# Performance work log

Hardware: AMD Instinct MI355X
Metric: run time of the kernel (lower is better)

The kernel has to match this reference:

```python
import jax, jax.numpy as jnp
import numpy as np

B, L, D, U = 8, 512, 256, 32

def setup_inputs() -> dict:
    key = jax.random.key(0)
    ks = jax.random.split(key, 6)
    g = lambda k, shape: jax.random.normal(k, shape, dtype=jnp.float32) * (2.0 / sum(shape)) ** 0.5
    return {
        "x": jax.random.normal(ks[0], (B, L, D), dtype=jnp.float32),
        "Wt": g(ks[1], (D, U)),
        "Wx": g(ks[2], (D, U)),
        "bh": jnp.zeros((U,), dtype=jnp.float32),
        "Wa": g(ks[3], (U, 1)),
        "ba": jnp.zeros((1,), dtype=jnp.float32),
    }

def reference(x, Wt, Wx, bh, Wa, ba):
    # q: [B,L,1,U], k: [B,1,L,U]
    q = jnp.einsum('bld,du->blu', x, Wt)[:, :, None, :]
    k = jnp.einsum('bld,du->blu', x, Wx)[:, None, :, :]
    beta = jnp.tanh(q + k + bh)                      # [B,L,L,U]
    alpha = jnp.einsum('bstu,u->bst', beta, Wa[:, 0]) + ba[0]  # [B,L,L]
    a = jax.nn.softmax(alpha, axis=-1)               # softmax over keys
    c_r = jnp.einsum('bst,btd->bsd', a, x)           # [B,L,D]
    return c_r
```

## Files before the change

kernel.cpp:

```cpp
#include <hip/hip_runtime.h>

#define B 8
#define L 512
#define D 256
#define U 32
#define ST 8
#define TR 32

__device__ __forceinline__ float tanh_fast(float z) {
    float e = __builtin_amdgcn_exp2f(z * 2.885390081777927f);
    return 1.f - 2.f * __builtin_amdgcn_rcpf(e + 1.f);
}

__global__ __launch_bounds__(256) void qk_kernel(
    const float* __restrict__ x,
    const float* __restrict__ Wt,
    const float* __restrict__ Wx,
    const float* __restrict__ bh,
    float* __restrict__ qb,
    float* __restrict__ kk)
{
    __shared__ float xs[TR][D + 1];
    const int row0 = blockIdx.x * TR;
    const int tid  = threadIdx.x;

    const float4* xg = (const float4*)(x + row0 * D);
    for (int i = tid; i < TR * D / 4; i += 256) {
        float4 v = xg[i];
        int r = i >> 6;
        int c = (i & 63) << 2;
        xs[r][c] = v.x; xs[r][c + 1] = v.y; xs[r][c + 2] = v.z; xs[r][c + 3] = v.w;
    }
    __syncthreads();

    const int r = tid >> 3;
    const int g = tid & 7;
    const float4* __restrict__ Wt4 = (const float4*)Wt;
    const float4* __restrict__ Wx4 = (const float4*)Wx;

    float4 qa = {0.f, 0.f, 0.f, 0.f};
    float4 ka = {0.f, 0.f, 0.f, 0.f};
    #pragma unroll 4
    for (int d = 0; d < D; ++d) {
        float  xv = xs[r][d];
        float4 wt = Wt4[d * 8 + g];
        float4 wx = Wx4[d * 8 + g];
        qa.x = fmaf(xv, wt.x, qa.x); qa.y = fmaf(xv, wt.y, qa.y);
        qa.z = fmaf(xv, wt.z, qa.z); qa.w = fmaf(xv, wt.w, qa.w);
        ka.x = fmaf(xv, wx.x, ka.x); ka.y = fmaf(xv, wx.y, ka.y);
        ka.z = fmaf(xv, wx.z, ka.z); ka.w = fmaf(xv, wx.w, ka.w);
    }
    float4 b4 = ((const float4*)bh)[g];
    qa.x += b4.x; qa.y += b4.y; qa.z += b4.z; qa.w += b4.w;

    const int row = row0 + r;
    ((float4*)qb)[row * 8 + g] = qa;
    ((float4*)kk)[row * 8 + g] = ka;
}

__global__ __launch_bounds__(256) void attn_kernel(
    const float* __restrict__ x,
    const float* __restrict__ qb,
    const float* __restrict__ kk,
    const float* __restrict__ Wa,
    const float* __restrict__ ba,
    float* __restrict__ out)
{
    const int blk = blockIdx.x;
    const int b   = blk >> 6;
    const int s0  = (blk & 63) * ST;
    const int tid = threadIdx.x;

    __shared__ float  a_sh[ST][L];
    __shared__ float4 part[3][ST][64];

    const float  ba0  = ba[0];
    const float* __restrict__ qrow = qb + (b * L + s0) * U;
    const float* __restrict__ kb   = kk + b * L * U;

    #pragma unroll 1
    for (int i = 0; i < 2; ++i) {
        const int t = tid + i * 256;
        float kv[U];
        const float4* k4 = (const float4*)(kb + t * U);
        #pragma unroll
        for (int c = 0; c < 8; ++c) {
            float4 v = k4[c];
            kv[4 * c] = v.x; kv[4 * c + 1] = v.y; kv[4 * c + 2] = v.z; kv[4 * c + 3] = v.w;
        }
        #pragma unroll 1
        for (int s = 0; s < ST; ++s) {
            const float* __restrict__ q = qrow + s * U;
            float acc = ba0;
            #pragma unroll
            for (int u = 0; u < U; ++u)
                acc = fmaf(tanh_fast(q[u] + kv[u]), Wa[u], acc);
            a_sh[s][t] = acc;
        }
    }
    __syncthreads();

    {
        const int wv = tid >> 6, ln = tid & 63;
        #pragma unroll 1
        for (int s = wv * 2; s < wv * 2 + 2; ++s) {
            float v[8];
            #pragma unroll
            for (int j = 0; j < 8; ++j) v[j] = a_sh[s][ln + 64 * j];
            float m = v[0];
            #pragma unroll
            for (int j = 1; j < 8; ++j) m = fmaxf(m, v[j]);
            #pragma unroll
            for (int off = 1; off < 64; off <<= 1) m = fmaxf(m, __shfl_xor(m, off));
            float e[8], sum = 0.f;
            #pragma unroll
            for (int j = 0; j < 8; ++j) { e[j] = __expf(v[j] - m); sum += e[j]; }
            #pragma unroll
            for (int off = 1; off < 64; off <<= 1) sum += __shfl_xor(sum, off);
            float inv = 1.f / sum;
            #pragma unroll
            for (int j = 0; j < 8; ++j) a_sh[s][ln + 64 * j] = e[j] * inv;
        }
    }
    __syncthreads();

    const int tq = tid >> 6;
    const int dg = tid & 63;
    const float4* __restrict__ x4 = (const float4*)(x + b * L * D);

    float4 acc[ST];
    #pragma unroll
    for (int s = 0; s < ST; ++s) acc[s] = make_float4(0.f, 0.f, 0.f, 0.f);

    #pragma unroll 1
    for (int jj = 0; jj < 32; ++jj) {
        const int tj = tq * 32 + jj;
        float4 av[ST];
        #pragma unroll
        for (int s = 0; s < ST; ++s) av[s] = ((const float4*)a_sh[s])[tj];
        #pragma unroll
        for (int c = 0; c < 4; ++c) {
            const int t = 4 * tj + c;
            float4 xv = x4[t * 64 + dg];
            #pragma unroll
            for (int s = 0; s < ST; ++s) {
                float a = (c == 0) ? av[s].x : (c == 1) ? av[s].y : (c == 2) ? av[s].z : av[s].w;
                acc[s].x = fmaf(a, xv.x, acc[s].x);
                acc[s].y = fmaf(a, xv.y, acc[s].y);
                acc[s].z = fmaf(a, xv.z, acc[s].z);
                acc[s].w = fmaf(a, xv.w, acc[s].w);
            }
        }
    }

    if (tq > 0) {
        #pragma unroll
        for (int s = 0; s < ST; ++s) part[tq - 1][s][dg] = acc[s];
    }
    __syncthreads();
    if (tq == 0) {
        float4* __restrict__ out4 = (float4*)out;
        #pragma unroll
        for (int s = 0; s < ST; ++s) {
            float4 p0 = part[0][s][dg], p1 = part[1][s][dg], p2 = part[2][s][dg];
            float4 r = acc[s];
            r.x += p0.x + p1.x + p2.x;
            r.y += p0.y + p1.y + p2.y;
            r.z += p0.z + p1.z + p2.z;
            r.w += p0.w + p1.w + p2.w;
            out4[(b * L + s0 + s) * 64 + dg] = r;
        }
    }
}

extern "C" void kernel_launch(void* const* d_in, const int* in_sizes, int n_in,
                              void* d_out, int out_size, void* d_ws, size_t ws_size,
                              hipStream_t stream)
{
    const float* x  = (const float*)d_in[0];
    const float* Wt = (const float*)d_in[1];
    const float* Wx = (const float*)d_in[2];
    const float* bh = (const float*)d_in[3];
    const float* Wa = (const float*)d_in[4];
    const float* ba = (const float*)d_in[5];
    float* out = (float*)d_out;

    float* qb = (float*)d_ws;
    float* kk = qb + B * L * U;

    qk_kernel<<<B * L / TR, 256, 0, stream>>>(x, Wt, Wx, bh, qb, kk);
    attn_kernel<<<B * (L / ST), 256, 0, stream>>>(x, qb, kk, Wa, ba, out);
}
```

Measured before the change: 121.6 us.

## Widen attention blocks to 512 threads and retile the qk projection

The attention kernel now launches 512 threads per block, so each thread computes one key's score, each of 8 waves handles one softmax row, and the weighted sum over x is split across 8 key slices that are reduced through shared memory. The qk projection kernel is retiled to 8 rows per block with one output unit per thread, giving 4x more blocks and scalar weight loads. The aim is more parallelism and latency hiding on the GPU. In exchange, the final cross-wave reduction grows from 3 to 7 partials, and the larger block size may reduce occupancy through register pressure.

Result: faster. 111.1 us (-8.7%).

```diff
diff --git a/kernel.cpp b/kernel.cpp
--- a/kernel.cpp
+++ b/kernel.cpp
@@ -5,7 +5,7 @@
 #define D 256
 #define U 32
 #define ST 8
-#define TR 32
+#define TR 8
 
 __device__ __forceinline__ float tanh_fast(float z) {
     float e = __builtin_amdgcn_exp2f(z * 2.885390081777927f);
@@ -25,6 +25,7 @@
     const int tid  = threadIdx.x;
 
     const float4* xg = (const float4*)(x + row0 * D);
+    #pragma unroll
     for (int i = tid; i < TR * D / 4; i += 256) {
         float4 v = xg[i];
         int r = i >> 6;
@@ -33,32 +34,22 @@
     }
     __syncthreads();
 
-    const int r = tid >> 3;
-    const int g = tid & 7;
-    const float4* __restrict__ Wt4 = (const float4*)Wt;
-    const float4* __restrict__ Wx4 = (const float4*)Wx;
+    const int r = tid >> 5;
+    const int u = tid & 31;
 
-    float4 qa = {0.f, 0.f, 0.f, 0.f};
-    float4 ka = {0.f, 0.f, 0.f, 0.f};
-    #pragma unroll 4
+    float qa = 0.f, ka = 0.f;
+    #pragma unroll 8
     for (int d = 0; d < D; ++d) {
-        float  xv = xs[r][d];
-        float4 wt = Wt4[d * 8 + g];
-        float4 wx = Wx4[d * 8 + g];
-        qa.x = fmaf(xv, wt.x, qa.x); qa.y = fmaf(xv, wt.y, qa.y);
-        qa.z = fmaf(xv, wt.z, qa.z); qa.w = fmaf(xv, wt.w, qa.w);
-        ka.x = fmaf(xv, wx.x, ka.x); ka.y = fmaf(xv, wx.y, ka.y);
-        ka.z = fmaf(xv, wx.z, ka.z); ka.w = fmaf(xv, wx.w, ka.w);
+        float xv = xs[r][d];
+        qa = fmaf(xv, Wt[d * U + u], qa);
+        ka = fmaf(xv, Wx[d * U + u], ka);
     }
-    float4 b4 = ((const float4*)bh)[g];
-    qa.x += b4.x; qa.y += b4.y; qa.z += b4.z; qa.w += b4.w;
-
     const int row = row0 + r;
-    ((float4*)qb)[row * 8 + g] = qa;
-    ((float4*)kk)[row * 8 + g] = ka;
+    qb[row * U + u] = qa + bh[u];
+    kk[row * U + u] = ka;
 }
 
-__global__ __launch_bounds__(256) void attn_kernel(
+__global__ __launch_bounds__(512) void attn_kernel(
     const float* __restrict__ x,
     const float* __restrict__ qb,
     const float* __restrict__ kk,
@@ -72,15 +63,14 @@
     const int tid = threadIdx.x;
 
     __shared__ float  a_sh[ST][L];
-    __shared__ float4 part[3][ST][64];
+    __shared__ float4 part[7][ST][64];
 
     const float  ba0  = ba[0];
     const float* __restrict__ qrow = qb + (b * L + s0) * U;
     const float* __restrict__ kb   = kk + b * L * U;
 
-    #pragma unroll 1
-    for (int i = 0; i < 2; ++i) {
-        const int t = tid + i * 256;
+    {
+        const int t = tid;
         float kv[U];
         const float4* k4 = (const float4*)(kb + t * U);
         #pragma unroll
@@ -101,26 +91,23 @@
     __syncthreads();
 
     {
-        const int wv = tid >> 6, ln = tid & 63;
-        #pragma unroll 1
-        for (int s = wv * 2; s < wv * 2 + 2; ++s) {
-            float v[8];
-            #pragma unroll
-            for (int j = 0; j < 8; ++j) v[j] = a_sh[s][ln + 64 * j];
-            float m = v[0];
-            #pragma unroll
-            for (int j = 1; j < 8; ++j) m = fmaxf(m, v[j]);
-            #pragma unroll
-            for (int off = 1; off < 64; off <<= 1) m = fmaxf(m, __shfl_xor(m, off));
-            float e[8], sum = 0.f;
-            #pragma unroll
-            for (int j = 0; j < 8; ++j) { e[j] = __expf(v[j] - m); sum += e[j]; }
-            #pragma unroll
-            for (int off = 1; off < 64; off <<= 1) sum += __shfl_xor(sum, off);
-            float inv = 1.f / sum;
-            #pragma unroll
-            for (int j = 0; j < 8; ++j) a_sh[s][ln + 64 * j] = e[j] * inv;
-        }
+        const int s = tid >> 6, ln = tid & 63;
+        float v[8];
+        #pragma unroll
+        for (int j = 0; j < 8; ++j) v[j] = a_sh[s][ln + 64 * j];
+        float m = v[0];
+        #pragma unroll
+        for (int j = 1; j < 8; ++j) m = fmaxf(m, v[j]);
+        #pragma unroll
+        for (int off = 1; off < 64; off <<= 1) m = fmaxf(m, __shfl_xor(m, off));
+        float e[8], sum = 0.f;
+        #pragma unroll
+        for (int j = 0; j < 8; ++j) { e[j] = __expf(v[j] - m); sum += e[j]; }
+        #pragma unroll
+        for (int off = 1; off < 64; off <<= 1) sum += __shfl_xor(sum, off);
+        float inv = 1.f / sum;
+        #pragma unroll
+        for (int j = 0; j < 8; ++j) a_sh[s][ln + 64 * j] = e[j] * inv;
     }
     __syncthreads();
 
@@ -132,9 +119,9 @@
     #pragma unroll
     for (int s = 0; s < ST; ++s) acc[s] = make_float4(0.f, 0.f, 0.f, 0.f);
 
-    #pragma unroll 1
-    for (int jj = 0; jj < 32; ++jj) {
-        const int tj = tq * 32 + jj;
+    #pragma unroll 2
+    for (int jj = 0; jj < 16; ++jj) {
+        const int tj = tq * 16 + jj;
         float4 av[ST];
         #pragma unroll
         for (int s = 0; s < ST; ++s) av[s] = ((const float4*)a_sh[s])[tj];
@@ -162,12 +149,12 @@
         float4* __restrict__ out4 = (float4*)out;
         #pragma unroll
         for (int s = 0; s < ST; ++s) {
-            float4 p0 = part[0][s][dg], p1 = part[1][s][dg], p2 = part[2][s][dg];
             float4 r = acc[s];
-            r.x += p0.x + p1.x + p2.x;
-            r.y += p0.y + p1.y + p2.y;
-            r.z += p0.z + p1.z + p2.z;
-            r.w += p0.w + p1.w + p2.w;
+            #pragma unroll
+            for (int w = 0; w < 7; ++w) {
+                float4 p = part[w][s][dg];
+                r.x += p.x; r.y += p.y; r.z += p.z; r.w += p.w;
+            }
             out4[(b * L + s0 + s) * 64 + dg] = r;
         }
     }
@@ -189,5 +176,5 @@
     float* kk = qb + B * L * U;
 
     qk_kernel<<<B * L / TR, 256, 0, stream>>>(x, Wt, Wx, bh, qb, kk);
-    attn_kernel<<<B * (L / ST), 256, 0, stream>>>(x, qb, kk, Wa, ba, out);
+    attn_kernel<<<B * (L / ST), 512, 0, stream>>>(x, qb, kk, Wa, ba, out);
 }
```
